# Kernel tuning notes

Measured on AMD Instinct MI355X. Metric: run time of the kernel, lower is better.

Reference implementation:

```python
import jax, jax.numpy as jnp
import numpy as np

NL = 8      # num layers (['self','cross']*4)
H = 8       # heads
EPS = 1e-5  # torch LayerNorm default


def _layernorm(x, g, b):
    mu = jnp.mean(x, axis=-1, keepdims=True)
    var = jnp.mean((x - mu) ** 2, axis=-1, keepdims=True)
    return (x - mu) * jax.lax.rsqrt(var + EPS) * g + b


def _encoder_layer(x, source, Wq, Wk, Wv, Wm, W1, W2, g1, b1, g2, b2):
    # x: [N, L, C], source: [N, S, C]
    N, L, C = x.shape
    D = C // H
    q = (x @ Wq).reshape(N, L, H, D)
    k = (source @ Wk).reshape(N, -1, H, D)
    v = (source @ Wv).reshape(N, -1, H, D)
    # naive full attention: explicit [N, L, S, H] scores (as in FullAttention)
    qk = jnp.einsum('nlhd,nshd->nlsh', q, k)
    A = jax.nn.softmax(qk * (1.0 / np.sqrt(D)), axis=2)
    msg = jnp.einsum('nlsh,nshd->nlhd', A, v).reshape(N, L, C)
    msg = _layernorm(msg @ Wm, g1, b1)
    m = jnp.concatenate([x, msg], axis=-1)          # [N, L, 2C]
    m = jax.nn.relu(m @ W1) @ W2                    # [N, L, C]
    m = _layernorm(m, g2, b2)
    return x + m


def _loftr(feat0, feat1, Wq, Wk, Wv, Wm, W1, W2, g1, b1, g2, b2):
    names = ['self', 'cross'] * 4
    for i, name in enumerate(names):
        p = (Wq[i], Wk[i], Wv[i], Wm[i], W1[i], W2[i], g1[i], b1[i], g2[i], b2[i])
        if name == 'self':
            feat0 = _encoder_layer(feat0, feat0, *p)
            feat1 = _encoder_layer(feat1, feat1, *p)
        else:  # cross; note feat0 is updated before being fed to feat1's layer
            feat0 = _encoder_layer(feat0, feat1, *p)
            feat1 = _encoder_layer(feat1, feat0, *p)
    return jnp.stack([feat0, feat1], axis=0)  # [2, N, L, C]


def setup_inputs() -> dict:
    key = jax.random.key(0)
    ks = jax.random.split(key, 10)
    N, L, C = 8, 1024, 768
    s = 1.0 / np.sqrt(C)       # xavier-ish scale for [C, C]
    s2 = 1.0 / np.sqrt(2 * C)  # for MLP fan-in 2C
    return {
        'feat0': jax.random.normal(ks[0], (N, L, C), jnp.float32),
        'feat1': jax.random.normal(ks[1], (N, L, C), jnp.float32),
        'Wq': jax.random.normal(ks[2], (NL, C, C), jnp.float32) * s,
        'Wk': jax.random.normal(ks[3], (NL, C, C), jnp.float32) * s,
        'Wv': jax.random.normal(ks[4], (NL, C, C), jnp.float32) * s,
        'Wm': jax.random.normal(ks[5], (NL, C, C), jnp.float32) * s,
        'W1': jax.random.normal(ks[6], (NL, 2 * C, 2 * C), jnp.float32) * s2,
        'W2': jax.random.normal(ks[7], (NL, 2 * C, C), jnp.float32) * s2,
        'g1': jnp.ones((NL, C), jnp.float32),
        'b1': jnp.zeros((NL, C), jnp.float32),
        'g2': jnp.ones((NL, C), jnp.float32),
        'b2': jnp.zeros((NL, C), jnp.float32),
    }


def reference(feat0, feat1, Wq, Wk, Wv, Wm, W1, W2, g1, b1, g2, b2):
    return _loftr(feat0, feat1, Wq, Wk, Wv, Wm, W1, W2, g1, b1, g2, b2)
```

## Files before the change

### kernel.cpp

```cpp
#include <hip/hip_runtime.h>
#include <hip/hip_bf16.h>

typedef __hip_bfloat16 bf16;
typedef __bf16 bf16x8 __attribute__((ext_vector_type(8)));
typedef float f32x4 __attribute__((ext_vector_type(4)));

#define AS1 __attribute__((address_space(1)))
#define AS3 __attribute__((address_space(3)))
__device__ __forceinline__ void gl_lds16(const void* g, void* l) {
    __builtin_amdgcn_global_load_lds((const AS1 void*)g, (AS3 void*)l, 16, 0, 0);
}

__device__ __forceinline__ float fexp2(float x) {
#if __has_builtin(__builtin_amdgcn_exp2f)
    return __builtin_amdgcn_exp2f(x);
#else
    return exp2f(x);
#endif
}

__device__ __forceinline__ int xcd_swz(int did, int nwg) {
    return (did & 7) * (nwg >> 3) + (did >> 3);
}


__global__ __launch_bounds__(256) void cvt_f32_bf16_k(const float* __restrict__ in, bf16* __restrict__ out,
                                                      int ostride, int total)
{
    int i = blockIdx.x * 256 + threadIdx.x;
    int e = i * 4;
    if (e >= total) return;
    int row = e / 768;
    int col = e - row * 768;
    const float4 f = *(const float4*)(in + e);
    bf16 o4[4];
    o4[0] = __float2bfloat16(f.x); o4[1] = __float2bfloat16(f.y);
    o4[2] = __float2bfloat16(f.z); o4[3] = __float2bfloat16(f.w);
    *(uint2*)(out + (size_t)row * ostride + col) = *(uint2*)o4;
}

__global__ void transpose_cvt_k(const float* __restrict__ in, bf16* __restrict__ out, int R, int C,
                                float scale, size_t lstride)
{
    __shared__ float t[32][33];
    const int tx = threadIdx.x, ty = threadIdx.y;
    in  += (size_t)blockIdx.z * R * C;
    out += (size_t)blockIdx.z * lstride;
    const int c0 = blockIdx.x * 32, r0 = blockIdx.y * 32;
    #pragma unroll
    for (int i = 0; i < 4; ++i)
        t[ty + i*8][tx] = in[(size_t)(r0 + ty + i*8) * C + c0 + tx];
    __syncthreads();
    #pragma unroll
    for (int i = 0; i < 4; ++i)
        out[(size_t)(c0 + ty + i*8) * R + r0 + tx] = __float2bfloat16(t[tx][ty + i*8] * scale);
}

template<int EPI>
__global__ __launch_bounds__(256) void gemm_bt_k(const bf16* __restrict__ A, int lda,
                                                 const bf16* __restrict__ BT, int K,
                                                 void* __restrict__ Cp, int ldc,
                                                 bf16* __restrict__ Ck, bf16* __restrict__ Cv,
                                                 const bf16* __restrict__ A2)
{
    __shared__ bf16 a_sm[3][4096];
    __shared__ bf16 b_sm[3][4096];
    const int tid = threadIdx.x;
    const int lane = tid & 63;
    const int wid = tid >> 6;
    const int wr = wid >> 1, wc = wid & 1;

    const int nwg = gridDim.x * gridDim.y;
    const int did = blockIdx.x + gridDim.x * blockIdx.y;
    const int wgid = xcd_swz(did, nwg);
    const int col0 = (wgid % gridDim.y) * 128;
    const int row0 = (wgid / gridDim.y) * 128;
    const int g = lane >> 4, r16 = lane & 15;

    if (EPI == 4 && col0 >= 768) A = A2;

    const int r4 = lane >> 2;
    const int sc = (lane & 3) ^ ((lane >> 3) & 3);
    const bf16* gA[2]; const bf16* gB[2]; int loff[2];
    #pragma unroll
    for (int i = 0; i < 2; ++i) {
        const int blk = wid*2 + i;
        gA[i] = A  + (size_t)(row0 + blk*16 + r4) * lda + sc*8;
        gB[i] = BT + (size_t)(col0 + blk*16 + r4) * K   + sc*8;
        loff[i] = blk * 512;
    }
    const int foff = r16*32 + ((g ^ ((r16 >> 1) & 3)) * 8);

    f32x4 acc[4][4];
    #pragma unroll
    for (int m = 0; m < 4; ++m)
        #pragma unroll
        for (int n = 0; n < 4; ++n)
            #pragma unroll
            for (int r = 0; r < 4; ++r) acc[m][n][r] = 0.f;

    #pragma unroll
    for (int i = 0; i < 2; ++i) {
        gl_lds16(gA[i],      &a_sm[0][loff[i]]);
        gl_lds16(gB[i],      &b_sm[0][loff[i]]);
    }
    #pragma unroll
    for (int i = 0; i < 2; ++i) {
        gl_lds16(gA[i] + 32, &a_sm[1][loff[i]]);
        gl_lds16(gB[i] + 32, &b_sm[1][loff[i]]);
    }

    int cur = 0, pre = 2;
    for (int k0 = 0; k0 < K; k0 += 32) {
        if (k0 + 32 < K) asm volatile("s_waitcnt vmcnt(4)" ::: "memory");
        else             asm volatile("s_waitcnt vmcnt(0)" ::: "memory");
        __builtin_amdgcn_s_barrier();
        if (k0 + 64 < K) {
            #pragma unroll
            for (int i = 0; i < 2; ++i) {
                gl_lds16(gA[i] + k0 + 64, &a_sm[pre][loff[i]]);
                gl_lds16(gB[i] + k0 + 64, &b_sm[pre][loff[i]]);
            }
        }
        bf16x8 af[4], bfr[4];
        #pragma unroll
        for (int m = 0; m < 4; ++m) af[m]  = *(const bf16x8*)&a_sm[cur][(wr*4 + m)*512 + foff];
        #pragma unroll
        for (int n = 0; n < 4; ++n) bfr[n] = *(const bf16x8*)&b_sm[cur][(wc*4 + n)*512 + foff];
        asm volatile("s_waitcnt lgkmcnt(0)" ::: "memory");
        __builtin_amdgcn_s_setprio(1);
        #pragma unroll
        for (int m = 0; m < 4; ++m)
            #pragma unroll
            for (int n = 0; n < 4; ++n)
                acc[m][n] = __builtin_amdgcn_mfma_f32_16x16x32_bf16(af[m], bfr[n], acc[m][n], 0, 0, 0);
        __builtin_amdgcn_s_setprio(0);
        cur = (cur == 2) ? 0 : cur + 1;
        pre = (pre == 2) ? 0 : pre + 1;
    }

    #pragma unroll
    for (int m = 0; m < 4; ++m) {
        const int orow = row0 + wr*64 + m*16 + g*4;
        #pragma unroll
        for (int n = 0; n < 4; ++n) {
            const int ocol = col0 + wc*64 + n*16 + r16;
            if (EPI == 4) {
                const int seg = ocol / 768;
                const int ci = ocol - seg*768;
                if (seg <= 1) {
                    bf16* dst = (seg == 0) ? (bf16*)Cp : Ck;
                    #pragma unroll
                    for (int r = 0; r < 4; ++r)
                        dst[(size_t)(orow + r)*768 + ci] = __float2bfloat16(acc[m][n][r]);
                } else {
                    const int nn = orow >> 10, ss = orow & 1023;
                    const int hh = ci / 96, dd = ci - hh * 96;
                    bf16 pk[4];
                    #pragma unroll
                    for (int r = 0; r < 4; ++r) pk[r] = __float2bfloat16(acc[m][n][r]);
                    *(uint2*)&Cv[(((size_t)nn*8 + hh)*96 + dd)*1024 + ss] = *(uint2*)pk;
                }
            } else {
                #pragma unroll
                for (int r = 0; r < 4; ++r) {
                    float v = acc[m][n][r];
                    if (EPI == 1) v = fmaxf(v, 0.f);
                    ((bf16*)Cp)[(size_t)(orow + r)*ldc + ocol] = __float2bfloat16(v);
                }
            }
        }
    }
}

__global__ __launch_bounds__(512) void attn_k(const bf16* __restrict__ qb, const bf16* __restrict__ kb,
                                              const bf16* __restrict__ vtb, bf16* __restrict__ msgb)
{
    __shared__ bf16 kv_sm[3][12*512];
    __shared__ bf16 p_sm_all[8][32][40];
    const int tid = threadIdx.x;
    const int lane = tid & 63;
    const int w = tid >> 6;
    const int g = lane >> 4, r16 = lane & 15;

    const int nwg = gridDim.x * gridDim.y;
    const int did = blockIdx.x + gridDim.x * blockIdx.y;
    const int wgid = xcd_swz(did, nwg);
    const int qx = wgid % gridDim.x;
    const int nh = wgid / gridDim.x;
    const int n = nh >> 3, h = nh & 7;
    const int q0 = qx * 256 + w * 32;

    bf16 (*p_sm)[40] = p_sm_all[w];

    const bf16* kbase = kb  + ((size_t)n*1024)*768 + (size_t)h*96;
    const bf16* vbase = vtb + ((size_t)(n*8 + h))*96*1024;

    bf16x8 aq[2][3];
    #pragma unroll
    for (int qh = 0; qh < 2; ++qh) {
        const size_t qoff = ((size_t)n*1024 + q0 + qh*16 + r16) * 768 + (size_t)h*96;
        #pragma unroll
        for (int c = 0; c < 3; ++c) aq[qh][c] = *(const bf16x8*)&qb[qoff + c*32 + g*8];
    }

    const int r4 = lane >> 2;
    const int sc = (lane & 3) ^ ((lane >> 3) & 3);
    const bf16* gsrc[2]; size_t gstep[2]; int dstoff[2];
    const int nissue = (w < 4) ? 2 : 1;
    #pragma unroll
    for (int jj = 0; jj < 2; ++jj) {
        const int issue = w + jj*8;
        if (issue < 6) {
            const int c = issue >> 1, kh = issue & 1;
            gsrc[jj]  = kbase + (size_t)(kh*16 + r4)*768 + c*32 + sc*8;
            gstep[jj] = 768;
        } else {
            gsrc[jj]  = vbase + (size_t)((issue-6)*16 + r4)*1024 + sc*8;
            gstep[jj] = 1;
        }
        dstoff[jj] = (issue < 12) ? issue * 512 : 0;
    }
    const int foff = r16*32 + ((g ^ ((r16 >> 1) & 3)) * 8);

    float m_run[2], l_run[2];
    #pragma unroll
    for (int qh = 0; qh < 2; ++qh) { m_run[qh] = -1e30f; l_run[qh] = 0.f; }
    f32x4 o[2][6];
    #pragma unroll
    for (int qg = 0; qg < 2; ++qg)
        #pragma unroll
        for (int f = 0; f < 6; ++f)
            #pragma unroll
            for (int r = 0; r < 4; ++r) o[qg][f][r] = 0.f;

    gl_lds16(gsrc[0], &kv_sm[0][dstoff[0]]);
    if (nissue == 2) gl_lds16(gsrc[1], &kv_sm[0][dstoff[1]]);
    gl_lds16(gsrc[0] + 32 * gstep[0], &kv_sm[1][dstoff[0]]);
    if (nissue == 2) gl_lds16(gsrc[1] + 32 * gstep[1], &kv_sm[1][dstoff[1]]);

    int cur = 0, pre = 2;
    for (int kt = 0; kt < 1024; kt += 32) {
        if (kt + 32 < 1024) {
            if (nissue == 2) asm volatile("s_waitcnt vmcnt(2)" ::: "memory");
            else             asm volatile("s_waitcnt vmcnt(1)" ::: "memory");
        } else {
            asm volatile("s_waitcnt vmcnt(0)" ::: "memory");
        }
        __builtin_amdgcn_s_barrier();
        if (kt + 64 < 1024) {
            gl_lds16(gsrc[0] + (size_t)(kt + 64) * gstep[0], &kv_sm[pre][dstoff[0]]);
            if (nissue == 2) gl_lds16(gsrc[1] + (size_t)(kt + 64) * gstep[1], &kv_sm[pre][dstoff[1]]);
        }
        const bf16* rd = kv_sm[cur];

        f32x4 s[2][2];
        #pragma unroll
        for (int kh = 0; kh < 2; ++kh)
            #pragma unroll
            for (int qh = 0; qh < 2; ++qh)
                #pragma unroll
                for (int r = 0; r < 4; ++r) s[kh][qh][r] = 0.f;
        __builtin_amdgcn_s_setprio(1);
        #pragma unroll
        for (int c = 0; c < 3; ++c) {
            bf16x8 ak0 = *(const bf16x8*)&rd[(c*2 + 0)*512 + foff];
            bf16x8 ak1 = *(const bf16x8*)&rd[(c*2 + 1)*512 + foff];
            s[0][0] = __builtin_amdgcn_mfma_f32_16x16x32_bf16(ak0, aq[0][c], s[0][0], 0, 0, 0);
            s[0][1] = __builtin_amdgcn_mfma_f32_16x16x32_bf16(ak0, aq[1][c], s[0][1], 0, 0, 0);
            s[1][0] = __builtin_amdgcn_mfma_f32_16x16x32_bf16(ak1, aq[0][c], s[1][0], 0, 0, 0);
            s[1][1] = __builtin_amdgcn_mfma_f32_16x16x32_bf16(ak1, aq[1][c], s[1][1], 0, 0, 0);
        }
        __builtin_amdgcn_s_setprio(0);

        float pmv[2], gr[2];
        #pragma unroll
        for (int qh = 0; qh < 2; ++qh) {
            float pm = fmaxf(fmaxf(fmaxf(s[0][qh][0], s[0][qh][1]), fmaxf(s[0][qh][2], s[0][qh][3])),
                             fmaxf(fmaxf(s[1][qh][0], s[1][qh][1]), fmaxf(s[1][qh][2], s[1][qh][3])));
            pm = fmaxf(pm, __shfl_xor(pm, 16, 64));
            pm = fmaxf(pm, __shfl_xor(pm, 32, 64));
            pmv[qh] = pm;
            gr[qh] = pm - m_run[qh];
        }
        if (__any(fmaxf(gr[0], gr[1]) > 8.0f)) {
            float alpha_c[2];
            #pragma unroll
            for (int qh = 0; qh < 2; ++qh) {
                float mn = fmaxf(m_run[qh], pmv[qh]);
                alpha_c[qh] = fexp2(m_run[qh] - mn);
                m_run[qh] = mn;
                l_run[qh] *= alpha_c[qh];
            }
            #pragma unroll
            for (int qg = 0; qg < 2; ++qg)
                #pragma unroll
                for (int r = 0; r < 4; ++r) {
                    float ar = __shfl(alpha_c[qg], g*4 + r, 64);
                    #pragma unroll
                    for (int f = 0; f < 6; ++f) o[qg][f][r] *= ar;
                }
        }
        #pragma unroll
        for (int qh = 0; qh < 2; ++qh) {
            bf16 pk0[4], pk1[4];
            float rs = 0.f;
            #pragma unroll
            for (int r = 0; r < 4; ++r) {
                float p0 = fexp2(s[0][qh][r] - m_run[qh]);
                float p1 = fexp2(s[1][qh][r] - m_run[qh]);
                rs += p0 + p1;
                pk0[r] = __float2bfloat16(p0);
                pk1[r] = __float2bfloat16(p1);
            }
            rs += __shfl_xor(rs, 16, 64);
            rs += __shfl_xor(rs, 32, 64);
            l_run[qh] += rs;
            *(uint2*)&p_sm[qh*16 + r16][g*4]      = *(uint2*)pk0;
            *(uint2*)&p_sm[qh*16 + r16][16 + g*4] = *(uint2*)pk1;
        }

        bf16x8 pa0 = *(const bf16x8*)&p_sm[r16][g*8];
        bf16x8 pa1 = *(const bf16x8*)&p_sm[16 + r16][g*8];
        __builtin_amdgcn_s_setprio(1);
        #pragma unroll
        for (int f = 0; f < 6; ++f) {
            bf16x8 bv = *(const bf16x8*)&rd[(6 + f)*512 + foff];
            o[0][f] = __builtin_amdgcn_mfma_f32_16x16x32_bf16(pa0, bv, o[0][f], 0, 0, 0);
            o[1][f] = __builtin_amdgcn_mfma_f32_16x16x32_bf16(pa1, bv, o[1][f], 0, 0, 0);
        }
        __builtin_amdgcn_s_setprio(0);
        asm volatile("s_waitcnt lgkmcnt(0)" ::: "memory");
        cur = (cur == 2) ? 0 : cur + 1;
        pre = (pre == 2) ? 0 : pre + 1;
    }

    float linv[2][4];
    #pragma unroll
    for (int qg = 0; qg < 2; ++qg)
        #pragma unroll
        for (int r = 0; r < 4; ++r)
            linv[qg][r] = 1.0f / __shfl(l_run[qg], g*4 + r, 64);

    #pragma unroll
    for (int qg = 0; qg < 2; ++qg) {
        const size_t obase = ((size_t)n*1024 + q0 + qg*16 + g*4) * 768 + (size_t)h*96;
        #pragma unroll
        for (int f = 0; f < 6; ++f)
            #pragma unroll
            for (int r = 0; r < 4; ++r)
                msgb[obase + (size_t)r*768 + f*16 + r16] = __float2bfloat16(o[qg][f][r] * linv[qg][r]);
    }
}

template<int MODE>
__global__ __launch_bounds__(256) void ln_k(const bf16* __restrict__ in, const float* __restrict__ g,
                                            const float* __restrict__ b, bf16* __restrict__ outc,
                                            float* __restrict__ x)
{
    const int row = blockIdx.x;
    const int tid = threadIdx.x;
    const bf16* rp = in + (size_t)row * 768;
    float v[3];
    #pragma unroll
    for (int j = 0; j < 3; ++j) v[j] = __bfloat162float(rp[tid + j*256]);
    float s  = v[0] + v[1] + v[2];
    float sq = v[0]*v[0] + v[1]*v[1] + v[2]*v[2];
    #pragma unroll
    for (int off = 32; off >= 1; off >>= 1) {
        s  += __shfl_xor(s,  off, 64);
        sq += __shfl_xor(sq, off, 64);
    }
    __shared__ float red[2][4];
    const int wid = tid >> 6;
    if ((tid & 63) == 0) { red[0][wid] = s; red[1][wid] = sq; }
    __syncthreads();
    const float S  = red[0][0] + red[0][1] + red[0][2] + red[0][3];
    const float SQ = red[1][0] + red[1][1] + red[1][2] + red[1][3];
    const float mu = S * (1.f/768.f);
    float var = SQ * (1.f/768.f) - mu*mu;
    var = fmaxf(var, 0.f);
    const float rs = rsqrtf(var + 1e-5f);
    #pragma unroll
    for (int j = 0; j < 3; ++j) {
        const int c = tid + j*256;
        const float y = (v[j] - mu) * rs * g[c] + b[c];
        if (MODE == 1) {
            outc[(size_t)row*1536 + 768 + c] = __float2bfloat16(y);
        } else {
            const float nx = x[(size_t)row*768 + c] + y;
            x[(size_t)row*768 + c] = nx;
            outc[(size_t)row*1536 + c] = __float2bfloat16(nx);
        }
    }
}

extern "C" void kernel_launch(void* const* d_in, const int* in_sizes, int n_in,
                              void* d_out, int out_size, void* d_ws, size_t ws_size,
                              hipStream_t stream)
{
    const float* feat0 = (const float*)d_in[0];
    const float* feat1 = (const float*)d_in[1];
    const float* Wq = (const float*)d_in[2];
    const float* Wk = (const float*)d_in[3];
    const float* Wv = (const float*)d_in[4];
    const float* Wm = (const float*)d_in[5];
    const float* W1 = (const float*)d_in[6];
    const float* W2 = (const float*)d_in[7];
    const float* g1 = (const float*)d_in[8];
    const float* b1 = (const float*)d_in[9];
    const float* g2 = (const float*)d_in[10];
    const float* b2 = (const float*)d_in[11];

    bf16 *wqkvT, *wmT, *w1T, *w2T, *concat0, *concat1, *qb, *kb, *vtb, *m1b, *t0b;
    auto plan = [&](int RB) -> size_t {
        char* p = (char*)d_ws;
        auto take = [&](size_t bytes) { char* q = p; p += (bytes + 255) & ~(size_t)255; return q; };
        wqkvT = (bf16*)take((size_t)8*2304*768*2);
        wmT  = (bf16*)take((size_t)8*768*768*2);
        w1T  = (bf16*)take((size_t)8*1536*1536*2);
        w2T  = (bf16*)take((size_t)8*768*1536*2);
        concat0 = (bf16*)take((size_t)8192*1536*2);
        concat1 = (bf16*)take((size_t)8192*1536*2);
        qb   = (bf16*)take((size_t)RB*768*2);
        kb   = (bf16*)take((size_t)RB*768*2);
        vtb  = (bf16*)take((size_t)RB*768*2);
        m1b  = (bf16*)take((size_t)RB*1536*2);
        t0b  = (bf16*)take((size_t)RB*768*2);
        return (size_t)(p - (char*)d_ws);
    };
    bool batched = plan(16384) <= ws_size;
    if (!batched) plan(8192);
    bf16* msgb = qb;

    float* x0 = (float*)d_out;
    float* x1 = x0 + (size_t)8192*768;

    hipMemcpyAsync(x0, feat0, (size_t)8192*768*4, hipMemcpyDeviceToDevice, stream);
    hipMemcpyAsync(x1, feat1, (size_t)8192*768*4, hipMemcpyDeviceToDevice, stream);

    const float s_qk = 0.14724444f;
    const dim3 tb(32, 8);
    const size_t QKV = (size_t)2304*768;
    transpose_cvt_k<<<dim3(24,24,8), tb, 0, stream>>>(Wq, wqkvT,            768, 768,  s_qk, QKV);
    transpose_cvt_k<<<dim3(24,24,8), tb, 0, stream>>>(Wk, wqkvT + 768*768,  768, 768,  1.0f, QKV);
    transpose_cvt_k<<<dim3(24,24,8), tb, 0, stream>>>(Wv, wqkvT + 1536*768, 768, 768,  1.0f, QKV);
    transpose_cvt_k<<<dim3(24,24,8), tb, 0, stream>>>(Wm, wmT, 768, 768,  1.0f, (size_t)768*768);
    transpose_cvt_k<<<dim3(48,48,8), tb, 0, stream>>>(W1, w1T, 1536, 1536, 1.0f, (size_t)1536*1536);
    transpose_cvt_k<<<dim3(24,48,8), tb, 0, stream>>>(W2, w2T, 1536, 768,  1.0f, (size_t)1536*768);

    const int total = 8192*768;
    cvt_f32_bf16_k<<<6144, 256, 0, stream>>>(feat0, concat0, 1536, total);
    cvt_f32_bf16_k<<<6144, 256, 0, stream>>>(feat1, concat1, 1536, total);

    auto encode = [&](float* x, bf16* cS, const bf16* cR, int i, int M) {
        const bf16* wl = wqkvT + (size_t)i * QKV;
        const int MT = M / 128;
        gemm_bt_k<4><<<dim3(MT,18), 256, 0, stream>>>(cS, 1536, wl, 768, qb, 768, kb, vtb, cR);
        attn_k<<<dim3(4, (M/1024)*8), 512, 0, stream>>>(qb, kb, vtb, msgb);
        gemm_bt_k<0><<<dim3(MT,6),  256, 0, stream>>>(msgb, 768, wmT + (size_t)i*768*768, 768,
                                                      t0b, 768, nullptr, nullptr, nullptr);
        ln_k<1><<<M, 256, 0, stream>>>(t0b, g1 + i*768, b1 + i*768, cS, nullptr);
        gemm_bt_k<1><<<dim3(MT,12), 256, 0, stream>>>(cS, 1536, w1T + (size_t)i*1536*1536, 1536,
                                                      m1b, 1536, nullptr, nullptr, nullptr);
        gemm_bt_k<0><<<dim3(MT,6),  256, 0, stream>>>(m1b, 1536, w2T + (size_t)i*768*1536, 1536,
                                                      t0b, 768, nullptr, nullptr, nullptr);
        ln_k<2><<<M, 256, 0, stream>>>(t0b, g2 + i*768, b2 + i*768, cS, x);
    };

    for (int i = 0; i < 8; ++i) {
        if ((i & 1) == 0) {
            if (batched) {
                encode(x0, concat0, concat0, i, 16384);
            } else {
                encode(x0, concat0, concat0, i, 8192);
                encode(x1, concat1, concat1, i, 8192);
            }
        } else {
            encode(x0, concat0, concat1, i, 8192);
            encode(x1, concat1, concat0, i, 8192);
        }
    }
}
```

Baseline: 3.399 ms.

## Shrink attention workgroups to 4 waves and pass P via shuffles

The attention kernel moves from 512-thread workgroups covering 256 queries to 256-thread workgroups covering 128 queries, with twice as many blocks in the grid. Each wave now issues three K/V tile loads per step instead of one or two. The per-wave LDS staging of the softmax probabilities is replaced by cross-lane shuffles that rearrange the P fragments directly into the MFMA A-operand layout. This removes the LDS writes and reads for P and may improve occupancy, but it doubles the total K/V traffic per head and adds many shuffle instructions.

```diff
diff --git a/kernel.cpp b/kernel.cpp
--- a/kernel.cpp
+++ b/kernel.cpp
@@ -173,11 +173,10 @@
     }
 }
 
-__global__ __launch_bounds__(512) void attn_k(const bf16* __restrict__ qb, const bf16* __restrict__ kb,
+__global__ __launch_bounds__(256) void attn_k(const bf16* __restrict__ qb, const bf16* __restrict__ kb,
                                               const bf16* __restrict__ vtb, bf16* __restrict__ msgb)
 {
     __shared__ bf16 kv_sm[3][12*512];
-    __shared__ bf16 p_sm_all[8][32][40];
     const int tid = threadIdx.x;
     const int lane = tid & 63;
     const int w = tid >> 6;
@@ -189,9 +188,7 @@
     const int qx = wgid % gridDim.x;
     const int nh = wgid / gridDim.x;
     const int n = nh >> 3, h = nh & 7;
-    const int q0 = qx * 256 + w * 32;
-
-    bf16 (*p_sm)[40] = p_sm_all[w];
+    const int q0 = qx * 128 + w * 32;
 
     const bf16* kbase = kb  + ((size_t)n*1024)*768 + (size_t)h*96;
     const bf16* vbase = vtb + ((size_t)(n*8 + h))*96*1024;
@@ -206,11 +203,10 @@
 
     const int r4 = lane >> 2;
     const int sc = (lane & 3) ^ ((lane >> 3) & 3);
-    const bf16* gsrc[2]; size_t gstep[2]; int dstoff[2];
-    const int nissue = (w < 4) ? 2 : 1;
-    #pragma unroll
-    for (int jj = 0; jj < 2; ++jj) {
-        const int issue = w + jj*8;
+    const bf16* gsrc[3]; size_t gstep[3]; int dstoff[3];
+    #pragma unroll
+    for (int jj = 0; jj < 3; ++jj) {
+        const int issue = w + jj*4;
         if (issue < 6) {
             const int c = issue >> 1, kh = issue & 1;
             gsrc[jj]  = kbase + (size_t)(kh*16 + r4)*768 + c*32 + sc*8;
@@ -219,9 +215,13 @@
             gsrc[jj]  = vbase + (size_t)((issue-6)*16 + r4)*1024 + sc*8;
             gstep[jj] = 1;
         }
-        dstoff[jj] = (issue < 12) ? issue * 512 : 0;
+        dstoff[jj] = issue * 512;
     }
     const int foff = r16*32 + ((g ^ ((r16 >> 1) & 3)) * 8);
+
+    const int sA = r16 + ((g & 1) << 5);
+    const int sB = sA + 16;
+    const bool khi = (g >= 2);
 
     float m_run[2], l_run[2];
     #pragma unroll
@@ -234,23 +234,20 @@
             #pragma unroll
             for (int r = 0; r < 4; ++r) o[qg][f][r] = 0.f;
 
-    gl_lds16(gsrc[0], &kv_sm[0][dstoff[0]]);
-    if (nissue == 2) gl_lds16(gsrc[1], &kv_sm[0][dstoff[1]]);
-    gl_lds16(gsrc[0] + 32 * gstep[0], &kv_sm[1][dstoff[0]]);
-    if (nissue == 2) gl_lds16(gsrc[1] + 32 * gstep[1], &kv_sm[1][dstoff[1]]);
+    #pragma unroll
+    for (int jj = 0; jj < 3; ++jj) gl_lds16(gsrc[jj], &kv_sm[0][dstoff[jj]]);
+    #pragma unroll
+    for (int jj = 0; jj < 3; ++jj) gl_lds16(gsrc[jj] + 32 * gstep[jj], &kv_sm[1][dstoff[jj]]);
 
     int cur = 0, pre = 2;
     for (int kt = 0; kt < 1024; kt += 32) {
-        if (kt + 32 < 1024) {
-            if (nissue == 2) asm volatile("s_waitcnt vmcnt(2)" ::: "memory");
-            else             asm volatile("s_waitcnt vmcnt(1)" ::: "memory");
-        } else {
-            asm volatile("s_waitcnt vmcnt(0)" ::: "memory");
-        }
+        if (kt + 32 < 1024) asm volatile("s_waitcnt vmcnt(3)" ::: "memory");
+        else                asm volatile("s_waitcnt vmcnt(0)" ::: "memory");
         __builtin_amdgcn_s_barrier();
         if (kt + 64 < 1024) {
-            gl_lds16(gsrc[0] + (size_t)(kt + 64) * gstep[0], &kv_sm[pre][dstoff[0]]);
-            if (nissue == 2) gl_lds16(gsrc[1] + (size_t)(kt + 64) * gstep[1], &kv_sm[pre][dstoff[1]]);
+            #pragma unroll
+            for (int jj = 0; jj < 3; ++jj)
+                gl_lds16(gsrc[jj] + (size_t)(kt + 64) * gstep[jj], &kv_sm[pre][dstoff[jj]]);
         }
         const bf16* rd = kv_sm[cur];
 
@@ -301,6 +298,7 @@
                     for (int f = 0; f < 6; ++f) o[qg][f][r] *= ar;
                 }
         }
+        bf16x8 pa[2];
         #pragma unroll
         for (int qh = 0; qh < 2; ++qh) {
             bf16 pk0[4], pk1[4];
@@ -316,18 +314,25 @@
             rs += __shfl_xor(rs, 16, 64);
             rs += __shfl_xor(rs, 32, 64);
             l_run[qh] += rs;
-            *(uint2*)&p_sm[qh*16 + r16][g*4]      = *(uint2*)pk0;
-            *(uint2*)&p_sm[qh*16 + r16][16 + g*4] = *(uint2*)pk1;
-        }
-
-        bf16x8 pa0 = *(const bf16x8*)&p_sm[r16][g*8];
-        bf16x8 pa1 = *(const bf16x8*)&p_sm[16 + r16][g*8];
+            uint2 P0 = *(uint2*)pk0, P1 = *(uint2*)pk1;
+            int a0x = __shfl((int)P0.x, sA, 64), a0y = __shfl((int)P0.y, sA, 64);
+            int a1x = __shfl((int)P1.x, sA, 64), a1y = __shfl((int)P1.y, sA, 64);
+            int b0x = __shfl((int)P0.x, sB, 64), b0y = __shfl((int)P0.y, sB, 64);
+            int b1x = __shfl((int)P1.x, sB, 64), b1y = __shfl((int)P1.y, sB, 64);
+            uint4 pau;
+            pau.x = (unsigned)(khi ? a1x : a0x);
+            pau.y = (unsigned)(khi ? a1y : a0y);
+            pau.z = (unsigned)(khi ? b1x : b0x);
+            pau.w = (unsigned)(khi ? b1y : b0y);
+            pa[qh] = *(bf16x8*)&pau;
+        }
+
         __builtin_amdgcn_s_setprio(1);
         #pragma unroll
         for (int f = 0; f < 6; ++f) {
             bf16x8 bv = *(const bf16x8*)&rd[(6 + f)*512 + foff];
-            o[0][f] = __builtin_amdgcn_mfma_f32_16x16x32_bf16(pa0, bv, o[0][f], 0, 0, 0);
-            o[1][f] = __builtin_amdgcn_mfma_f32_16x16x32_bf16(pa1, bv, o[1][f], 0, 0, 0);
+            o[0][f] = __builtin_amdgcn_mfma_f32_16x16x32_bf16(pa[0], bv, o[0][f], 0, 0, 0);
+            o[1][f] = __builtin_amdgcn_mfma_f32_16x16x32_bf16(pa[1], bv, o[1][f], 0, 0, 0);
         }
         __builtin_amdgcn_s_setprio(0);
         asm volatile("s_waitcnt lgkmcnt(0)" ::: "memory");
@@ -457,7 +462,7 @@
         const bf16* wl = wqkvT + (size_t)i * QKV;
         const int MT = M / 128;
         gemm_bt_k<4><<<dim3(MT,18), 256, 0, stream>>>(cS, 1536, wl, 768, qb, 768, kb, vtb, cR);
-        attn_k<<<dim3(4, (M/1024)*8), 512, 0, stream>>>(qb, kb, vtb, msgb);
+        attn_k<<<dim3(8, (M/1024)*8), 256, 0, stream>>>(qb, kb, vtb, msgb);
         gemm_bt_k<0><<<dim3(MT,6),  256, 0, stream>>>(msgb, 768, wmT + (size_t)i*768*768, 768,
                                                       t0b, 768, nullptr, nullptr, nullptr);
         ln_k<1><<<M, 256, 0, stream>>>(t0b, g1 + i*768, b1 + i*768, cS, nullptr);
```

After: 3.651 ms. 1.07x slower.
